# Kernel optimization log

Measured on AMD Instinct MI355X. Metric: run time of the kernel, lower is better.

The kernel has to match this reference:

```python
import jax, jax.numpy as jnp
import numpy as np

WINDOW_SHAPE = (12, 12, 32)  # (win_x, win_y, win_z)
GROUP_SIZE = 69
SHIFT = True


def setup_inputs() -> dict:
    rng = np.random.default_rng(0)
    Z, Y, X = 32, 512, 512
    batch_size = 8
    counts = [250000 + 37 * i + (i % 3) for i in range(batch_size)]  # non-multiples of GROUP_SIZE
    grid = Z * Y * X
    rows = []
    for b, n in enumerate(counts):
        lin = rng.choice(grid, size=n, replace=False)  # unique voxels per batch -> unique sort keys
        z = lin // (Y * X)
        y = (lin // X) % Y
        x = lin % X
        rows.append(np.stack([np.full(n, b), z, y, x], axis=1))
    coords = jnp.asarray(np.concatenate(rows, axis=0).astype(np.int32))
    return {"coords": coords, "batch_size": batch_size, "sparse_shape": (Z, Y, X)}


def reference(coords, batch_size, sparse_shape):
    g = GROUP_SIZE
    win_x, win_y, win_z = WINDOW_SHAPE
    sz, sy, sx = sparse_shape
    coords = coords.astype(jnp.int32)
    N = coords.shape[0]

    # ---- per-batch counts and (padded) start offsets (coords sorted by batch id) ----
    counts = jnp.bincount(coords[:, 0], length=batch_size).astype(jnp.int32)
    bs = jnp.concatenate([jnp.zeros(1, jnp.int32), jnp.cumsum(counts).astype(jnp.int32)])
    counts_p = ((counts + g - 1) // g) * g  # rounded up to multiple of group_size
    bsp = jnp.concatenate([jnp.zeros(1, jnp.int32), jnp.cumsum(counts_p).astype(jnp.int32)])
    Np = int(bsp[-1])  # padded total (eager; output length is data-dependent by construction)

    # ---- win2flat: original index -> padded position ----
    pb = coords[:, 0]  # batch of each point
    win2flat = jnp.arange(N, dtype=jnp.int32) + (bsp[:-1] - bs[:-1])[pb]

    # ---- flat2win: padded position -> original index (vectorized form of the torch loop) ----
    j = jnp.arange(Np, dtype=jnp.int32)
    b = (jnp.searchsorted(bsp, j, side='right') - 1).astype(jnp.int32)  # batch of padded pos
    off = bsp[b] - bs[b]
    num = counts[b]
    num_p = counts_p[b]
    r = num % g
    has_pad = num != num_p
    tail_start = jnp.where(has_pad, bsp[b + 1] - g + r, bsp[b + 1])
    in_tail = j >= tail_start
    multi_group = num_p != g
    val_multi = j - g - off                       # copy previous group's entries
    t = j - tail_start
    val_single = bs[b] + (t % jnp.maximum(num, 1))  # wrap-around repeat of batch elements
    flat2win = jnp.where(in_tail, jnp.where(multi_group, val_multi, val_single), j - off)

    # ---- window sort keys (win_version == 'v2') ----
    shift_x, shift_y, shift_z = (win_x // 2, win_y // 2, win_z // 2) if SHIFT else (0, 0, 0)
    mwx = int(np.ceil(sx / win_x) + 1)
    mwy = int(np.ceil(sy / win_y) + 1)
    mwz = int(np.ceil(sz / win_z) + 1)
    mps = mwx * mwy * mwz  # max windows per sample

    x = coords[:, 3] + shift_x
    y = coords[:, 2] + shift_y
    z = coords[:, 1] + shift_z
    wx, wy, wz = x // win_x, y // win_y, z // win_z
    cx, cy, cz = x % win_x, y % win_y, z % win_z

    bwi_x = coords[:, 0] * mps + wx * (mwy * mwz) + wy * mwz + wz
    bwi_y = coords[:, 0] * mps + wy * (mwx * mwz) + wx * mwz + wz

    vol = win_x * win_y * win_z
    vx = bwi_x * vol + cx * (win_y * win_z) + cy * win_z + cz
    vy = bwi_y * vol + cy * (win_x * win_z) + cx * win_z + cz

    x_map = jnp.argsort(vx).astype(jnp.int32)
    y_map = jnp.argsort(vy).astype(jnp.int32)

    return flat2win, win2flat, x_map, y_map
```

## Files before the change

### kernel.cpp

```cpp
#include <hip/hip_runtime.h>
#include <stdint.h>

#define G       69
#define BATCH   8
#define MPS     3872
#define VOL     4608
#define NBUK    1089
#define NB2     2178
#define B_WORDS 4096
#define BT      1024
#define CT      1024
#define CBLK    35
#define ST      1024
#define RT      512
#define NBLK    256

#define C_COUNTS 0
#define C_BS     8
#define C_CP     17
#define C_BSP    25

#define BSWZ(w) ((w) ^ (((w) >> 4) & 15))

__device__ __forceinline__ void keys_from_coord(int4 c, unsigned& kx, unsigned& ky) {
    int b  = c.x;
    int zz = c.y + 16;
    int yy = c.z + 6;
    int xx = c.w + 6;
    int wx = xx / 12, cx = xx - wx*12;
    int wy = yy / 12, cy = yy - wy*12;
    int wz = zz >> 5, cz = zz & 31;
    int bwx = b*MPS + wx*88 + wy*2 + wz;
    int bwy = b*MPS + wy*88 + wx*2 + wz;
    kx = (unsigned)(bwx*VOL + cx*384 + cy*32 + cz);
    ky = (unsigned)(bwy*VOL + cy*384 + cx*32 + cz);
}

__device__ __forceinline__ unsigned wave_iscan(unsigned x, int lane) {
    #pragma unroll
    for (int d = 1; d < 64; d <<= 1) {
        unsigned u = __shfl_up(x, d, 64);
        if (lane >= d) x += u;
    }
    return x;
}

__global__ __launch_bounds__(BT) void hist_kernel(const int4* __restrict__ coords, int N, int chunk,
                            int* __restrict__ ctrl, unsigned* __restrict__ histMat) {
    __shared__ unsigned h[NB2];
    __shared__ int hb[BATCH];
    int t = threadIdx.x, blk = blockIdx.x;
    for (int k = t; k < NB2; k += BT) h[k] = 0u;
    if (t < BATCH) hb[t] = 0;
    __syncthreads();
    int start = blk * chunk;
    int end   = min(start + chunk, N);
    int c0=0,c1=0,c2=0,c3=0,c4=0,c5=0,c6=0,c7=0;
    for (int i = start + t; i < end; i += BT) {
        int4 c = coords[i];
        int b = c.x;
        c0 += (b==0); c1 += (b==1); c2 += (b==2); c3 += (b==3);
        c4 += (b==4); c5 += (b==5); c6 += (b==6); c7 += (b==7);
        unsigned kx, ky;
        keys_from_coord(c, kx, ky);
        atomicAdd(&h[kx >> 17], 1u);
        atomicAdd(&h[NBUK + (ky >> 17)], 1u);
    }
    if (c0) atomicAdd(&hb[0],c0);  if (c1) atomicAdd(&hb[1],c1);
    if (c2) atomicAdd(&hb[2],c2);  if (c3) atomicAdd(&hb[3],c3);
    if (c4) atomicAdd(&hb[4],c4);  if (c5) atomicAdd(&hb[5],c5);
    if (c6) atomicAdd(&hb[6],c6);  if (c7) atomicAdd(&hb[7],c7);
    __syncthreads();
    for (int k = t; k < NB2; k += BT) histMat[(size_t)blk * NB2 + k] = h[k];
    if (t < BATCH && hb[t]) atomicAdd(&ctrl[C_COUNTS + t], hb[t]);
}

__global__ __launch_bounds__(CT) void colscan_kernel(unsigned* __restrict__ histMat,
                               unsigned* __restrict__ totals) {
    __shared__ unsigned part[16][64];
    int t = threadIdx.x;
    int lane = t & 63, wid = t >> 6;
    int col = blockIdx.x * 64 + lane;
    unsigned v[16];
    unsigned s = 0;
    if (col < NB2) {
        #pragma unroll
        for (int u = 0; u < 16; u++) v[u] = histMat[(size_t)(wid*16 + u) * NB2 + col];
        #pragma unroll
        for (int u = 0; u < 16; u++) s += v[u];
    }
    part[wid][lane] = s;
    __syncthreads();
    if (wid == 0) {
        unsigned run = 0;
        #pragma unroll
        for (int w = 0; w < 16; w++) {
            unsigned tmp = part[w][lane];
            part[w][lane] = run;
            run += tmp;
        }
        if (col < NB2) totals[col] = run;
    }
    __syncthreads();
    if (col < NB2) {
        unsigned excl = part[wid][lane];
        #pragma unroll
        for (int u = 0; u < 16; u++) {
            histMat[(size_t)(wid*16 + u) * NB2 + col] = excl;
            excl += v[u];
        }
    }
}

__global__ __launch_bounds__(ST) void scan_kernel(int* __restrict__ ctrl,
                            const unsigned* __restrict__ totals,
                            unsigned* __restrict__ recStart) {
    __shared__ unsigned warpsum[ST/64];
    __shared__ unsigned s_carry;
    int t = threadIdx.x;
    int lane = t & 63, wid = t >> 6;
    if (t == 0) s_carry = 0u;
    __syncthreads();
    for (int base = 0; base < NB2; base += ST) {
        int idx = base + t;
        unsigned v = (idx < NB2) ? totals[idx] : 0u;
        unsigned x = wave_iscan(v, lane);
        if (lane == 63) warpsum[wid] = x;
        __syncthreads();
        if (wid == 0) {
            unsigned v2 = (lane < ST/64) ? warpsum[lane] : 0u;
            unsigned x2 = wave_iscan(v2, lane);
            if (lane < ST/64) warpsum[lane] = x2;
        }
        __syncthreads();
        unsigned excl = s_carry + (wid ? warpsum[wid-1] : 0u) + x - v;
        unsigned roundTot = warpsum[ST/64 - 1];
        if (idx < NB2) recStart[idx] = excl;
        __syncthreads();
        if (t == 0) s_carry += roundTot;
        __syncthreads();
    }
    if (t == 0) {
        recStart[NB2] = s_carry;
        int bs = 0, bsp = 0;
        ctrl[C_BS] = 0; ctrl[C_BSP] = 0;
        for (int b = 0; b < BATCH; b++) {
            int n  = ctrl[C_COUNTS + b];
            int np = ((n + G - 1) / G) * G;
            ctrl[C_CP + b] = np;
            bs += n; bsp += np;
            ctrl[C_BS + b + 1]  = bs;
            ctrl[C_BSP + b + 1] = bsp;
        }
    }
}

__global__ __launch_bounds__(BT) void bin_kernel(const int4* __restrict__ coords, int N, int chunk, int Np,
                           const int* __restrict__ ctrl,
                           const unsigned* __restrict__ recStart,
                           const unsigned* __restrict__ histMat,
                           uint2* __restrict__ rec,
                           int* __restrict__ w2f,
                           int* __restrict__ f2w) {
    __shared__ unsigned cur[NB2];
    __shared__ int s_off[BATCH];
    __shared__ int s_bs[BATCH+1], s_bsp[BATCH+1], s_cnt[BATCH], s_cp[BATCH];
    int t = threadIdx.x, blk = blockIdx.x;
    if (t < BATCH) {
        s_off[t] = ctrl[C_BSP+t] - ctrl[C_BS+t];
        s_cnt[t] = ctrl[C_COUNTS+t];
        s_cp[t]  = ctrl[C_CP+t];
    }
    if (t < BATCH+1) { s_bs[t] = ctrl[C_BS+t]; s_bsp[t] = ctrl[C_BSP+t]; }
    for (int k = t; k < NB2; k += BT)
        cur[k] = recStart[k] + histMat[(size_t)blk * NB2 + k];
    __syncthreads();
    int start = blk * chunk;
    int end   = min(start + chunk, N);
    for (int i = start + t; i < end; i += BT) {
        int4 c = coords[i];
        w2f[i] = i + s_off[c.x];
        unsigned kx, ky;
        keys_from_coord(c, kx, ky);
        unsigned px = atomicAdd(&cur[kx >> 17], 1u);
        rec[px] = make_uint2(kx, (unsigned)i);
        unsigned py = atomicAdd(&cur[NBUK + (ky >> 17)], 1u);
        rec[py] = make_uint2(ky, (unsigned)i);
    }
    int gs = (int)gridDim.x * BT;
    for (int j = blk*BT + t; j < Np; j += gs) {
        int b = 0;
        #pragma unroll
        for (int k = 1; k < BATCH; k++) b += (j >= s_bsp[k]);
        int off  = s_bsp[b] - s_bs[b];
        int num  = s_cnt[b], nump = s_cp[b];
        int r    = num % G;
        int tail_start = (num != nump) ? (s_bsp[b+1] - G + r) : s_bsp[b+1];
        int v;
        if (j < tail_start)       v = j - off;
        else if (nump != G)       v = j - G - off;
        else { int tt = j - tail_start; int m = num > 0 ? num : 1; v = s_bs[b] + tt % m; }
        f2w[j] = v;
    }
}

__global__ __launch_bounds__(RT) void rank_kernel(const uint2* __restrict__ rec,
                            const unsigned* __restrict__ recStart, int N,
                            int* __restrict__ xmap, int* __restrict__ ymap) {
    int b = blockIdx.x;
    unsigned start = recStart[b], end = recStart[b+1];
    int cnt = (int)(end - start);
    if (cnt == 0) return;
    int map = (b >= NBUK);
    __shared__ unsigned bits[B_WORDS];
    __shared__ unsigned short pref[B_WORDS];
    __shared__ unsigned wsum[RT/64];
    int t = threadIdx.x;
    #pragma unroll
    for (int k = 0; k < B_WORDS/RT; k++) bits[t + RT*k] = 0u;
    __syncthreads();
    for (int j = t; j < cnt; j += RT) {
        unsigned key = rec[start + j].x;
        unsigned local = key & 131071u;
        atomicOr(&bits[BSWZ(local >> 5)], 1u << (local & 31));
    }
    __syncthreads();
    int base = t * (B_WORDS/RT);
    unsigned w[B_WORDS/RT];
    unsigned s = 0;
    #pragma unroll
    for (int k = 0; k < B_WORDS/RT; k++) { w[k] = bits[BSWZ(base + k)]; s += __popc(w[k]); }
    int lane = t & 63, wid = t >> 6;
    unsigned x = wave_iscan(s, lane);
    if (lane == 63) wsum[wid] = x;
    __syncthreads();
    unsigned add = 0;
    #pragma unroll
    for (int q = 0; q < RT/64 - 1; q++) add += (wid > q) ? wsum[q] : 0u;
    unsigned excl = add + x - s;
    #pragma unroll
    for (int k = 0; k < B_WORDS/RT; k++) {
        pref[BSWZ(base + k)] = (unsigned short)excl;
        excl += __popc(w[k]);
    }
    __syncthreads();
    int* __restrict__ out = map ? ymap : xmap;
    unsigned rankBase = start - (map ? (unsigned)N : 0u);
    for (int j = t; j < cnt; j += RT) {
        uint2 r = rec[start + j];
        unsigned local = r.x & 131071u;
        unsigned wd = local >> 5, bt = local & 31u;
        unsigned sw = BSWZ(wd);
        unsigned rank = rankBase + (unsigned)pref[sw] + __popc(bits[sw] & ((1u << bt) - 1u));
        out[rank] = (int)r.y;
    }
}

extern "C" void kernel_launch(void* const* d_in, const int* in_sizes, int n_in,
                              void* d_out, int out_size, void* d_ws, size_t ws_size,
                              hipStream_t stream) {
    const int* coords = (const int*)d_in[0];
    int N  = in_sizes[0] / 4;
    int Np = out_size - 3 * N;
    int chunk = (N + NBLK - 1) / NBLK;

    char* ws = (char*)d_ws;
    int*      ctrl     = (int*)(ws + 0);
    unsigned* totals   = (unsigned*)(ws + 256);
    unsigned* recStart = (unsigned*)(ws + 8968);
    unsigned* histMat  = (unsigned*)(ws + 17696);
    uint2*    rec      = (uint2*)(ws + 2247968);

    int* out  = (int*)d_out;
    int* f2w  = out;
    int* w2f  = out + Np;
    int* xmap = out + Np + N;
    int* ymap = out + Np + 2*N;

    hipMemsetAsync(ctrl, 0, 256, stream);

    hist_kernel<<<NBLK, BT, 0, stream>>>((const int4*)coords, N, chunk, ctrl, histMat);
    colscan_kernel<<<CBLK, CT, 0, stream>>>(histMat, totals);
    scan_kernel<<<1, ST, 0, stream>>>(ctrl, totals, recStart);
    bin_kernel<<<NBLK, BT, 0, stream>>>((const int4*)coords, N, chunk, Np, ctrl, recStart, histMat, rec, w2f, f2w);
    rank_kernel<<<NB2, RT, 0, stream>>>(rec, recStart, N, xmap, ymap);
}
```

Baseline: 143.7 us.

## Move flat2win fill into rank kernel and stage bucket records in LDS

The flat2win computation moves out of the binning kernel and into the rank kernel, which has more blocks (2178 of 512 threads) to spread the writes over. The rank kernel also keeps up to 1536 records per bucket in shared memory on the first pass, so the second pass reads them from LDS instead of reloading them from global memory. The extra 12 KB of LDS per block may lower occupancy in the rank kernel, and the flat2win loop now runs before the bucket work in every block.

```diff
diff --git a/kernel.cpp b/kernel.cpp
--- a/kernel.cpp
+++ b/kernel.cpp
@@ -8,6 +8,7 @@
 #define NBUK    1089
 #define NB2     2178
 #define B_WORDS 4096
+#define STAGE   1536
 #define BT      1024
 #define CT      1024
 #define CBLK    35
@@ -155,23 +156,17 @@
     }
 }
 
-__global__ __launch_bounds__(BT) void bin_kernel(const int4* __restrict__ coords, int N, int chunk, int Np,
+__global__ __launch_bounds__(BT) void bin_kernel(const int4* __restrict__ coords, int N, int chunk,
                            const int* __restrict__ ctrl,
                            const unsigned* __restrict__ recStart,
                            const unsigned* __restrict__ histMat,
                            uint2* __restrict__ rec,
-                           int* __restrict__ w2f,
-                           int* __restrict__ f2w) {
+                           int* __restrict__ w2f) {
     __shared__ unsigned cur[NB2];
     __shared__ int s_off[BATCH];
-    __shared__ int s_bs[BATCH+1], s_bsp[BATCH+1], s_cnt[BATCH], s_cp[BATCH];
     int t = threadIdx.x, blk = blockIdx.x;
-    if (t < BATCH) {
+    if (t < BATCH)
         s_off[t] = ctrl[C_BSP+t] - ctrl[C_BS+t];
-        s_cnt[t] = ctrl[C_COUNTS+t];
-        s_cp[t]  = ctrl[C_CP+t];
-    }
-    if (t < BATCH+1) { s_bs[t] = ctrl[C_BS+t]; s_bsp[t] = ctrl[C_BSP+t]; }
     for (int k = t; k < NB2; k += BT)
         cur[k] = recStart[k] + histMat[(size_t)blk * NB2 + k];
     __syncthreads();
@@ -187,8 +182,24 @@
         unsigned py = atomicAdd(&cur[NBUK + (ky >> 17)], 1u);
         rec[py] = make_uint2(ky, (unsigned)i);
     }
-    int gs = (int)gridDim.x * BT;
-    for (int j = blk*BT + t; j < Np; j += gs) {
+}
+
+__global__ __launch_bounds__(RT) void rank_kernel(const uint2* __restrict__ rec,
+                            const unsigned* __restrict__ recStart, int N, int Np,
+                            const int* __restrict__ ctrl,
+                            int* __restrict__ xmap, int* __restrict__ ymap,
+                            int* __restrict__ f2w) {
+    __shared__ int s_bs[BATCH+1], s_bsp[BATCH+1], s_cnt[BATCH], s_cp[BATCH];
+    __shared__ unsigned bits[B_WORDS];
+    __shared__ unsigned short pref[B_WORDS];
+    __shared__ uint2 stage[STAGE];
+    __shared__ unsigned wsum[RT/64];
+    int t = threadIdx.x;
+    if (t < BATCH)   { s_cnt[t] = ctrl[C_COUNTS+t]; s_cp[t] = ctrl[C_CP+t]; }
+    if (t < BATCH+1) { s_bs[t]  = ctrl[C_BS+t];     s_bsp[t] = ctrl[C_BSP+t]; }
+    __syncthreads();
+    int gs = (int)gridDim.x * RT;
+    for (int j = blockIdx.x*RT + t; j < Np; j += gs) {
         int b = 0;
         #pragma unroll
         for (int k = 1; k < BATCH; k++) b += (j >= s_bsp[k]);
@@ -202,26 +213,18 @@
         else { int tt = j - tail_start; int m = num > 0 ? num : 1; v = s_bs[b] + tt % m; }
         f2w[j] = v;
     }
-}
-
-__global__ __launch_bounds__(RT) void rank_kernel(const uint2* __restrict__ rec,
-                            const unsigned* __restrict__ recStart, int N,
-                            int* __restrict__ xmap, int* __restrict__ ymap) {
     int b = blockIdx.x;
     unsigned start = recStart[b], end = recStart[b+1];
     int cnt = (int)(end - start);
     if (cnt == 0) return;
     int map = (b >= NBUK);
-    __shared__ unsigned bits[B_WORDS];
-    __shared__ unsigned short pref[B_WORDS];
-    __shared__ unsigned wsum[RT/64];
-    int t = threadIdx.x;
     #pragma unroll
     for (int k = 0; k < B_WORDS/RT; k++) bits[t + RT*k] = 0u;
     __syncthreads();
     for (int j = t; j < cnt; j += RT) {
-        unsigned key = rec[start + j].x;
-        unsigned local = key & 131071u;
+        uint2 r = rec[start + j];
+        if (j < STAGE) stage[j] = r;
+        unsigned local = r.x & 131071u;
         atomicOr(&bits[BSWZ(local >> 5)], 1u << (local & 31));
     }
     __syncthreads();
@@ -247,7 +250,7 @@
     int* __restrict__ out = map ? ymap : xmap;
     unsigned rankBase = start - (map ? (unsigned)N : 0u);
     for (int j = t; j < cnt; j += RT) {
-        uint2 r = rec[start + j];
+        uint2 r = (j < STAGE) ? stage[j] : rec[start + j];
         unsigned local = r.x & 131071u;
         unsigned wd = local >> 5, bt = local & 31u;
         unsigned sw = BSWZ(wd);
@@ -282,6 +285,6 @@
     hist_kernel<<<NBLK, BT, 0, stream>>>((const int4*)coords, N, chunk, ctrl, histMat);
     colscan_kernel<<<CBLK, CT, 0, stream>>>(histMat, totals);
     scan_kernel<<<1, ST, 0, stream>>>(ctrl, totals, recStart);
-    bin_kernel<<<NBLK, BT, 0, stream>>>((const int4*)coords, N, chunk, Np, ctrl, recStart, histMat, rec, w2f, f2w);
-    rank_kernel<<<NB2, RT, 0, stream>>>(rec, recStart, N, xmap, ymap);
-}
+    bin_kernel<<<NBLK, BT, 0, stream>>>((const int4*)coords, N, chunk, ctrl, recStart, histMat, rec, w2f);
+    rank_kernel<<<NB2, RT, 0, stream>>>(rec, recStart, N, Np, ctrl, xmap, ymap, f2w);
+}
```

Measured after the change: 147.3 us. 1.03x slower.
